# Kernel optimization log

Measured on AMD Instinct MI355X. Metric: run time of the kernel, lower is better.

Reference implementation:

```python
import jax, jax.numpy as jnp
import numpy as np
from jax import lax

NUM_HEADS = 4
OUT_DIM = 384
HEAD_DIM = 96
STRIDE_Q = 2
STRIDE_KV = 2
EPS = 1e-6
SCALE = HEAD_DIM ** -0.5


def _layernorm(x, g, b):
    m = jnp.mean(x, axis=-1, keepdims=True)
    v = jnp.mean((x - m) ** 2, axis=-1, keepdims=True)
    return (x - m) * lax.rsqrt(v + EPS) * g + b


def _pool(x, w, h, wd, stride):
    # x: [B, nh, N, hd] -> depthwise conv stride-s -> [B, nh, oh*ow, hd]
    B, nh, N, hd = x.shape
    x = x.reshape(B * nh, h, wd, hd).transpose(0, 3, 1, 2)  # NCHW
    y = lax.conv_general_dilated(x, w, (stride, stride), ((1, 1), (1, 1)),
                                 feature_group_count=hd)
    oh, ow = y.shape[2], y.shape[3]
    y = y.reshape(B, nh, hd, oh * ow).transpose(0, 1, 3, 2)
    return y, (oh, ow)


def _add_rel_pos(attn, q, q_size, k_size, rel_h, rel_w):
    qh, qw = q_size
    kh, kw = k_size
    B, nh, _, hd = q.shape
    qhr = max(kh / qh, 1.0); khr = max(qh / kh, 1.0)
    dh = (jnp.arange(qh)[:, None] * qhr - jnp.arange(kh)[None, :] * khr
          + (kh - 1) * khr).astype(jnp.int32)
    qwr = max(kw / qw, 1.0); kwr = max(qw / kw, 1.0)
    dw = (jnp.arange(qw)[:, None] * qwr - jnp.arange(kw)[None, :] * kwr
          + (kw - 1) * kwr).astype(jnp.int32)
    Reh = rel_h[dh]  # [qh, kh, hd]
    Rew = rel_w[dw]  # [qw, kw, hd]
    qr = q.reshape(B, nh, qh, qw, hd)
    eh = jnp.einsum('byhwc,hkc->byhwk', qr, Reh)
    ew = jnp.einsum('byhwc,wkc->byhwk', qr, Rew)
    a = attn.reshape(B, nh, qh, qw, kh, kw) + eh[..., :, None] + ew[..., None, :]
    return a.reshape(B, nh, qh * qw, kh * kw)


def setup_inputs() -> dict:
    key = jax.random.key(0)
    ks = jax.random.split(key, 8)
    B, N, IN_DIM = 16, 3136, 192
    return {
        'hidden_states': jax.random.normal(ks[0], (B, N, IN_DIM), jnp.float32),
        'qkv_w': jax.random.normal(ks[1], (IN_DIM, 3 * OUT_DIM), jnp.float32) * 0.02,
        'qkv_b': jax.random.normal(ks[2], (3 * OUT_DIM,), jnp.float32) * 0.02,
        'pool_q_w': jax.random.normal(ks[3], (HEAD_DIM, 1, 3, 3), jnp.float32) * 0.1,
        'pool_k_w': jax.random.normal(ks[4], (HEAD_DIM, 1, 3, 3), jnp.float32) * 0.1,
        'pool_v_w': jax.random.normal(ks[5], (HEAD_DIM, 1, 3, 3), jnp.float32) * 0.1,
        'ln_q_g': jnp.ones((HEAD_DIM,), jnp.float32),
        'ln_q_b': jnp.zeros((HEAD_DIM,), jnp.float32),
        'ln_k_g': jnp.ones((HEAD_DIM,), jnp.float32),
        'ln_k_b': jnp.zeros((HEAD_DIM,), jnp.float32),
        'ln_v_g': jnp.ones((HEAD_DIM,), jnp.float32),
        'ln_v_b': jnp.zeros((HEAD_DIM,), jnp.float32),
        'rel_h': jax.random.normal(ks[6], (55, HEAD_DIM), jnp.float32) * 0.02,
        'rel_w': jax.random.normal(ks[7], (55, HEAD_DIM), jnp.float32) * 0.02,
        'height': 56,
        'width': 56,
    }


def reference(hidden_states, qkv_w, qkv_b, pool_q_w, pool_k_w, pool_v_w,
              ln_q_g, ln_q_b, ln_k_g, ln_k_b, ln_v_g, ln_v_b,
              rel_h, rel_w, height, width):
    B, N, _ = hidden_states.shape
    qkv = (hidden_states @ qkv_w + qkv_b).reshape(B, N, 3, NUM_HEADS, HEAD_DIM)
    qkv = qkv.transpose(2, 0, 3, 1, 4)  # [3, B, nh, N, hd]
    q, k, v = qkv[0], qkv[1], qkv[2]

    q, q_size = _pool(q, pool_q_w, height, width, STRIDE_Q)
    q = _layernorm(q, ln_q_g, ln_q_b)
    k, k_size = _pool(k, pool_k_w, height, width, STRIDE_KV)
    k = _layernorm(k, ln_k_g, ln_k_b)
    v, _ = _pool(v, pool_v_w, height, width, STRIDE_KV)
    v = _layernorm(v, ln_v_g, ln_v_b)

    attn = jnp.einsum('bhqd,bhkd->bhqk', q * SCALE, k)
    attn = _add_rel_pos(attn, q, q_size, k_size, rel_h, rel_w)
    attn = jax.nn.softmax(attn, axis=-1)
    out = jnp.einsum('bhqk,bhkd->bhqd', attn, v)
    out = out + q  # residual pooling (no cls token)
    out = out.transpose(0, 2, 1, 3).reshape(B, -1, OUT_DIM)
    return out
```

## Files before the change

kernel.cpp:

```cpp
#include <hip/hip_runtime.h>

#define DEVI __device__ __forceinline__

typedef __attribute__((ext_vector_type(8))) short short8;
typedef __attribute__((ext_vector_type(4))) short short4v;
typedef __attribute__((ext_vector_type(4))) float f32x4;
typedef __attribute__((ext_vector_type(4))) unsigned int u32x4;

#define ATTN_SCALE 0.10206207261596575f
#define LOG2E      1.4426950408889634f
#define KSCALE     (ATTN_SCALE * LOG2E)

DEVI unsigned short f2bf(float f){
  unsigned u = __float_as_uint(f);
  u += 0x7fff + ((u >> 16) & 1);
  return (unsigned short)(u >> 16);
}
DEVI float bf2f(unsigned short h){ return __uint_as_float(((unsigned)h) << 16); }

DEVI void gload16(const void* g, void* l){
  __builtin_amdgcn_global_load_lds((const __attribute__((address_space(1))) void*)g,
                                   (__attribute__((address_space(3))) void*)l, 16, 0, 0);
}

DEVI f32x4 mfma16(short8 a, short8 b, f32x4 c){
  return __builtin_amdgcn_mfma_f32_16x16x32_bf16(a, b, c, 0, 0, 0);
}

DEVI short8 pack_bf8s(const float* p, float s){
  float4 a = *(const float4*)p, b = *(const float4*)(p + 4);
  short8 r;
  r[0] = f2bf(a.x * s); r[1] = f2bf(a.y * s); r[2] = f2bf(a.z * s); r[3] = f2bf(a.w * s);
  r[4] = f2bf(b.x * s); r[5] = f2bf(b.y * s); r[6] = f2bf(b.z * s); r[7] = f2bf(b.w * s);
  return r;
}

__global__ __launch_bounds__(256) void k_convert(const float4* __restrict__ hs4,
    const float* __restrict__ w, unsigned short* __restrict__ hsb,
    unsigned short* __restrict__ wt){
  const int stride = gridDim.x * 256;
  const int t0 = blockIdx.x * 256 + threadIdx.x;
  const int n4 = (50176 * 192) / 4;
  for (int i = t0; i < n4; i += stride){
    float4 v = hs4[i];
    uint2 p;
    p.x = (unsigned)f2bf(v.x) | ((unsigned)f2bf(v.y) << 16);
    p.y = (unsigned)f2bf(v.z) | ((unsigned)f2bf(v.w) << 16);
    ((uint2*)hsb)[i] = p;
  }
  for (int i = t0; i < 192 * 1152; i += stride){
    int k = i / 1152, n = i - k * 1152;
    wt[n * 192 + k] = f2bf(w[i]);
  }
}

__global__ __launch_bounds__(256) void k_gemm(const unsigned short* __restrict__ A,
    const unsigned short* __restrict__ Bt,
    const float* __restrict__ bias, unsigned short* __restrict__ C){
  __shared__ unsigned short sA[2][128 * 64];
  __shared__ unsigned short sB[2][128 * 64];
  const int bid = (blockIdx.x & 7) * 441 + (blockIdx.x >> 3);
  const int bn = bid % 9, bm = bid / 9;
  const int tid = threadIdx.x, w = tid >> 6, l = tid & 63;
  const int wr = (w >> 1) * 64, wc = (w & 1) * 64;
  const int l15 = l & 15, l4 = l >> 4;
  const f32x4 z4 = {0.f, 0.f, 0.f, 0.f};
  f32x4 acc[4][4];
#pragma unroll
  for (int i = 0; i < 4; ++i)
#pragma unroll
    for (int j = 0; j < 4; ++j) acc[i][j] = z4;

  auto stage = [&](int kk, int buf){
    const int k0 = kk * 64;
#pragma unroll
    for (int i = 0; i < 4; ++i){
      const int ib = (w * 4 + i) << 10;
      const int Lb = ib + (l << 4);
      const int r  = Lb >> 7;
      const int g  = ((Lb >> 4) & 7) ^ (r & 7);
      gload16((const char*)A  + (size_t)(bm * 128 + r) * 384 + k0 * 2 + g * 16, (char*)sA[buf] + ib);
      gload16((const char*)Bt + (size_t)(bn * 128 + r) * 384 + k0 * 2 + g * 16, (char*)sB[buf] + ib);
    }
  };

  stage(0, 0);
  __syncthreads();
  for (int kk = 0; kk < 3; ++kk){
    const int buf = kk & 1;
    if (kk < 2) stage(kk + 1, buf ^ 1);
#pragma unroll
    for (int ks = 0; ks < 2; ++ks){
      short8 av[4], bv[4];
#pragma unroll
      for (int mf = 0; mf < 4; ++mf){
        const int r = wr + mf * 16 + l15;
        const int slot = (ks * 4 + l4) ^ (r & 7);
        av[mf] = *(const short8*)(sA[buf] + r * 64 + slot * 8);
      }
#pragma unroll
      for (int nf = 0; nf < 4; ++nf){
        const int r = wc + nf * 16 + l15;
        const int slot = (ks * 4 + l4) ^ (r & 7);
        bv[nf] = *(const short8*)(sB[buf] + r * 64 + slot * 8);
      }
#pragma unroll
      for (int mf = 0; mf < 4; ++mf)
#pragma unroll
        for (int nf = 0; nf < 4; ++nf)
          acc[mf][nf] = mfma16(av[mf], bv[nf], acc[mf][nf]);
    }
    if (kk < 2) __syncthreads();
  }
#pragma unroll
  for (int nf = 0; nf < 4; ++nf){
    const int col = bn * 128 + wc + nf * 16 + l15;
    const float bv = bias[col];
#pragma unroll
    for (int mf = 0; mf < 4; ++mf)
#pragma unroll
      for (int reg = 0; reg < 4; ++reg){
        const int row = bm * 128 + wr + mf * 16 + l4 * 4 + reg;
        C[(size_t)row * 1152 + col] = f2bf(acc[mf][nf][reg] + bv);
      }
  }
}

__global__ __launch_bounds__(384) void k_pool_ln(const unsigned short* __restrict__ qkv,
    const float* __restrict__ wq, const float* __restrict__ wk, const float* __restrict__ wv,
    const float* __restrict__ gq, const float* __restrict__ bq,
    const float* __restrict__ gk, const float* __restrict__ bk,
    const float* __restrict__ gv, const float* __restrict__ bv,
    unsigned short* __restrict__ qp, unsigned short* __restrict__ kp,
    unsigned short* __restrict__ vpt, float* __restrict__ qpf){
  __shared__ float swt[9 * 96];
  __shared__ float sg[96], sb[96];
  __shared__ float sbuf[28 * 96];
  const int bid = blockIdx.x;
  const int oy = bid % 28, h = (bid / 28) & 3, b = (bid / 112) & 15, which = bid / 1792;
  const float* wsel = which == 0 ? wq : (which == 1 ? wk : wv);
  const float* gsel = which == 0 ? gq : (which == 1 ? gk : gv);
  const float* bsel = which == 0 ? bq : (which == 1 ? bk : bv);
  const int tid = threadIdx.x;
  for (int i = tid; i < 864; i += 384){
    const int d = i / 9, t = i - d * 9;
    swt[t * 96 + d] = wsel[i];
  }
  if (tid < 96){ sg[tid] = gsel[tid]; sb[tid] = bsel[tid]; }
  __syncthreads();

  const int colbase = which * 384 + h * 96;
  if (tid < 336){
    const int ox = tid / 12, d0 = (tid - ox * 12) * 8;
    float acc[8] = {0.f,0.f,0.f,0.f,0.f,0.f,0.f,0.f};
#pragma unroll
    for (int ky = 0; ky < 3; ++ky){
      const int iy = oy * 2 + ky - 1;
      if ((unsigned)iy >= 56u) continue;
      const unsigned short* rowp = qkv + (size_t)(b * 3136 + iy * 56) * 1152 + colbase + d0;
#pragma unroll
      for (int kx = 0; kx < 3; ++kx){
        const int ix = ox * 2 + kx - 1;
        if ((unsigned)ix >= 56u) continue;
        const u32x4 raw = *(const u32x4*)(rowp + (size_t)ix * 1152);
        const float* wv8 = swt + (ky * 3 + kx) * 96 + d0;
        const float4 wa = *(const float4*)wv8;
        const float4 wb = *(const float4*)(wv8 + 4);
        acc[0] += __uint_as_float(raw[0] << 16)         * wa.x;
        acc[1] += __uint_as_float(raw[0] & 0xffff0000u) * wa.y;
        acc[2] += __uint_as_float(raw[1] << 16)         * wa.z;
        acc[3] += __uint_as_float(raw[1] & 0xffff0000u) * wa.w;
        acc[4] += __uint_as_float(raw[2] << 16)         * wb.x;
        acc[5] += __uint_as_float(raw[2] & 0xffff0000u) * wb.y;
        acc[6] += __uint_as_float(raw[3] << 16)         * wb.z;
        acc[7] += __uint_as_float(raw[3] & 0xffff0000u) * wb.w;
      }
    }
    *(float4*)(sbuf + ox * 96 + d0)     = *(float4*)acc;
    *(float4*)(sbuf + ox * 96 + d0 + 4) = *(float4*)(acc + 4);
  }
  __syncthreads();

  const int grp = tid >> 3, l8 = tid & 7;
  if (grp < 28){
    const int ox = grp, d0 = l8 * 12;
    float x[12];
    *(float4*)x       = *(const float4*)(sbuf + ox * 96 + d0);
    *(float4*)(x + 4) = *(const float4*)(sbuf + ox * 96 + d0 + 4);
    *(float4*)(x + 8) = *(const float4*)(sbuf + ox * 96 + d0 + 8);
    float s = 0.f, ss = 0.f;
#pragma unroll
    for (int j = 0; j < 12; ++j){ s += x[j]; ss += x[j] * x[j]; }
#pragma unroll
    for (int d = 1; d < 8; d <<= 1){ s += __shfl_xor(s, d); ss += __shfl_xor(ss, d); }
    const float mean = s * (1.f / 96.f);
    const float var  = ss * (1.f / 96.f) - mean * mean;
    const float rstd = rsqrtf(var + 1e-6f);
    const int n = oy * 28 + ox;
    const size_t bh = (size_t)(b * 4 + h);
    float y[12];
#pragma unroll
    for (int j = 0; j < 12; ++j)
      y[j] = (x[j] - mean) * rstd * sg[d0 + j] + sb[d0 + j];
    if (which == 0){
      const size_t idx = (bh * 784 + n) * 96 + d0;
#pragma unroll
      for (int c = 0; c < 3; ++c){
        short4v p;
        p[0] = (short)f2bf(y[c*4]);   p[1] = (short)f2bf(y[c*4+1]);
        p[2] = (short)f2bf(y[c*4+2]); p[3] = (short)f2bf(y[c*4+3]);
        *(short4v*)(qp + idx + c * 4) = p;
        *(float4*)(qpf + idx + c * 4) = *(const float4*)(y + c * 4);
      }
    } else if (which == 1){
      const size_t idx = (bh * 784 + n) * 160;
#pragma unroll
      for (int c = 0; c < 3; ++c){
        short4v p;
        p[0] = (short)f2bf(y[c*4]   * KSCALE); p[1] = (short)f2bf(y[c*4+1] * KSCALE);
        p[2] = (short)f2bf(y[c*4+2] * KSCALE); p[3] = (short)f2bf(y[c*4+3] * KSCALE);
        *(short4v*)(kp + idx + d0 + c * 4) = p;
      }
      short8 oh;
#pragma unroll
      for (int jj = 0; jj < 8; ++jj){
        const int pcol = 96 + l8 * 8 + jj;
        unsigned short v = 0;
        if (pcol == 96 + oy)  v = 0x3F80;
        if (pcol == 128 + ox) v = 0x3F80;
        oh[jj] = (short)v;
      }
      *(short8*)(kp + idx + 96 + l8 * 8) = oh;
    } else {
#pragma unroll
      for (int j = 0; j < 12; ++j)
        vpt[(bh * 96 + d0 + j) * 784 + n] = f2bf(y[j]);
    }
  }
}

__global__ __launch_bounds__(512, 4) void k_attn(
    const unsigned short* __restrict__ qp, const unsigned short* __restrict__ kp,
    const unsigned short* __restrict__ vpt, const float* __restrict__ qpf,
    const float* __restrict__ relh, const float* __restrict__ relw,
    float* __restrict__ out){
  __shared__ unsigned short sK[2][64 * 160];
  __shared__ unsigned short sV[96 * 64];

  const int s = blockIdx.x, xcd = s & 7, slot = s >> 3;
  const int bh = xcd * 8 + slot / 7, qb = slot - (slot / 7) * 7;
  const int b = bh >> 2, h = bh & 3;
  const int tid = threadIdx.x, w = tid >> 6, l = tid & 63;
  const int l15 = l & 15, l4 = l >> 4;
  const size_t baseq = (size_t)bh * 784 * 96;
  const size_t basek = (size_t)bh * 784 * 160;
  const f32x4 z4 = {0.f, 0.f, 0.f, 0.f};
  const int qrl = w * 16 + l15;
  int q_l = qb * 128 + qrl; if (q_l > 783) q_l = 783;

  auto stageK = [&](int t, int buf){
#pragma unroll
    for (int r = 0; r < 3; ++r){
      if (r == 2 && tid >= 256) continue;
      const int off = r * 8192 + (tid << 4);
      const int row = ((off >> 6) * 205) >> 10;
      const int rem = off - row * 320;
      const int sg_ = (rem >> 4) ^ (row & 3);
      int kr = t * 64 + row; if (kr > 783) kr = 783;
      gload16((const char*)kp + ((size_t)(basek + (size_t)kr * 160) + sg_ * 8) * 2,
              (char*)sK[buf] + off);
    }
  };
  short8 vreg[2];
  auto loadV = [&](int t){
    if (tid < 384){
#pragma unroll
      for (int i = 0; i < 2; ++i){
        const int off = (tid * 2 + i) << 4;
        const int r = off >> 7;
        const int g = ((off >> 4) & 7) ^ (r & 7);
        int koff = t * 64 + g * 8; if (koff + 8 > 784) koff = 0;
        vreg[i] = *(const short8*)(vpt + (size_t)(bh * 96 + r) * 784 + koff);
      }
    }
  };
  auto writeV = [&](){
    if (tid < 384){
#pragma unroll
      for (int i = 0; i < 2; ++i)
        *(short8*)((char*)sV + ((tid * 2 + i) << 4)) = vreg[i];
    }
  };

  stageK(0, 0);
  loadV(0);

  short8 qf[5];
#pragma unroll
  for (int ks = 0; ks < 3; ++ks)
    qf[ks] = *(const short8*)(qp + baseq + (size_t)q_l * 96 + ks * 32 + l4 * 8);

  const int hh = (q_l * 2341) >> 16;
  const int ww = q_l - hh * 28;
  const int h0 = (qb * 128) / 28;

  {
    unsigned short* sGh = sK[1];
    unsigned short* sGw = sK[1] + 4096;
    f32x4 gh[3] = {z4, z4, z4}, gw[4] = {z4, z4, z4, z4};
#pragma unroll
    for (int nf = 0; nf < 3; ++nf){
      int j = h0 + nf * 16 + l15; if (j > 54) j = 54;
#pragma unroll
      for (int ks = 0; ks < 3; ++ks)
        gh[nf] = mfma16(pack_bf8s(relh + j * 96 + ks * 32 + l4 * 8, LOG2E), qf[ks], gh[nf]);
    }
#pragma unroll
    for (int nf = 0; nf < 4; ++nf){
      int j = nf * 16 + l15; if (j > 54) j = 54;
#pragma unroll
      for (int ks = 0; ks < 3; ++ks)
        gw[nf] = mfma16(pack_bf8s(relw + j * 96 + ks * 32 + l4 * 8, LOG2E), qf[ks], gw[nf]);
    }
    if (l4 == 0){
      *(short4v*)(sGh + qrl * 32 + 28) = (short4v)0;
      *(short4v*)(sGw + qrl * 32 + 28) = (short4v)0;
    }
#pragma unroll
    for (int nf = 0; nf < 3; ++nf)
#pragma unroll
      for (int reg = 0; reg < 4; ++reg){
        const int j = h0 + nf * 16 + l4 * 4 + reg;
        const int kh = hh + 27 - j;
        if ((unsigned)kh < 28u) sGh[qrl * 32 + kh] = f2bf(gh[nf][reg]);
      }
#pragma unroll
    for (int nf = 0; nf < 4; ++nf)
#pragma unroll
      for (int reg = 0; reg < 4; ++reg){
        const int j = nf * 16 + l4 * 4 + reg;
        const int kw = ww + 27 - j;
        if ((unsigned)kw < 28u) sGw[qrl * 32 + kw] = f2bf(gw[nf][reg]);
      }
    qf[3] = *(const short8*)(sGh + qrl * 32 + l4 * 8);
    qf[4] = *(const short8*)(sGw + qrl * 32 + l4 * 8);
  }

  float m = -1e30f, lsum = 0.f;
  f32x4 acc[6];
#pragma unroll
  for (int i = 0; i < 6; ++i) acc[i] = z4;

  writeV();
  __syncthreads();

  for (int kt = 0; kt < 13; ++kt){
    const int cur = kt & 1;
    if (kt < 12){ loadV(kt + 1); stageK(kt + 1, cur ^ 1); }

    f32x4 sfr[4] = {z4, z4, z4, z4};
#pragma unroll
    for (int ks = 0; ks < 5; ++ks){
#pragma unroll
      for (int nf = 0; nf < 4; ++nf){
        const int r = nf * 16 + l15;
        const int sl = (ks * 4 + l4) ^ (r & 3);
        const short8 kb = *(const short8*)(sK[cur] + r * 160 + sl * 8);
        sfr[nf] = mfma16(kb, qf[ks], sfr[nf]);
      }
    }
    if (kt == 12){
      const f32x4 m30 = {-1e30f, -1e30f, -1e30f, -1e30f};
      sfr[1] = m30; sfr[2] = m30; sfr[3] = m30;
    }

    float mx;
    {
      float a0 = fmaxf(fmaxf(sfr[0][0], sfr[0][1]), fmaxf(sfr[0][2], sfr[0][3]));
      float a1 = fmaxf(fmaxf(sfr[1][0], sfr[1][1]), fmaxf(sfr[1][2], sfr[1][3]));
      float a2 = fmaxf(fmaxf(sfr[2][0], sfr[2][1]), fmaxf(sfr[2][2], sfr[2][3]));
      float a3 = fmaxf(fmaxf(sfr[3][0], sfr[3][1]), fmaxf(sfr[3][2], sfr[3][3]));
      mx = fmaxf(fmaxf(a0, a1), fmaxf(a2, a3));
    }
    mx = fmaxf(mx, __shfl_xor(mx, 16));
    mx = fmaxf(mx, __shfl_xor(mx, 32));
    const float mn = fmaxf(m, mx);
    const float al = exp2f(m - mn);
    m = mn;
    float sum;
    {
#pragma unroll
      for (int nf = 0; nf < 4; ++nf)
#pragma unroll
        for (int reg = 0; reg < 4; ++reg)
          sfr[nf][reg] = exp2f(sfr[nf][reg] - mn);
      float s0 = (sfr[0][0] + sfr[0][1]) + (sfr[0][2] + sfr[0][3]);
      float s1 = (sfr[1][0] + sfr[1][1]) + (sfr[1][2] + sfr[1][3]);
      float s2 = (sfr[2][0] + sfr[2][1]) + (sfr[2][2] + sfr[2][3]);
      float s3 = (sfr[3][0] + sfr[3][1]) + (sfr[3][2] + sfr[3][3]);
      sum = (s0 + s1) + (s2 + s3);
    }
    sum += __shfl_xor(sum, 16);
    sum += __shfl_xor(sum, 32);
    lsum = lsum * al + sum;

    __syncthreads();

    unsigned short* sPp = sK[cur];
#pragma unroll
    for (int nf = 0; nf < 4; ++nf){
      short4v p4;
      p4[0] = (short)f2bf(sfr[nf][0]); p4[1] = (short)f2bf(sfr[nf][1]);
      p4[2] = (short)f2bf(sfr[nf][2]); p4[3] = (short)f2bf(sfr[nf][3]);
      char* dst = (char*)sPp + qrl * 128 + (((nf * 2 + (l4 >> 1)) ^ (l15 & 7)) << 4) + ((l4 & 1) << 3);
      *(short4v*)dst = p4;
    }
#pragma unroll
    for (int i = 0; i < 6; ++i)
#pragma unroll
      for (int reg = 0; reg < 4; ++reg)
        acc[i][reg] *= al;

#pragma unroll
    for (int ks = 0; ks < 2; ++ks){
      const short8 pb = *(const short8*)((char*)sPp + qrl * 128 + (((ks * 4 + l4) ^ (l15 & 7)) << 4));
#pragma unroll
      for (int nf = 0; nf < 6; ++nf){
        const int r = nf * 16 + l15;
        const int sl = (ks * 4 + l4) ^ (r & 7);
        const short8 vb = *(const short8*)(sV + r * 64 + sl * 8);
        acc[nf] = mfma16(vb, pb, acc[nf]);
      }
    }

    if (kt < 12){
      __syncthreads();
      writeV();
      __syncthreads();
    }
  }

  const int qg = qb * 128 + qrl;
  if (qg < 784){
    const float rcp = 1.f / lsum;
    const float* qrow = qpf + baseq + (size_t)qg * 96;
    float* orow = out + ((size_t)b * 784 + qg) * 384 + h * 96;
#pragma unroll
    for (int nf = 0; nf < 6; ++nf)
#pragma unroll
      for (int reg = 0; reg < 4; ++reg){
        const int d = nf * 16 + l4 * 4 + reg;
        orow[d] = acc[nf][reg] * rcp + qrow[d];
      }
  }
}

extern "C" void kernel_launch(void* const* d_in, const int* in_sizes, int n_in,
                              void* d_out, int out_size, void* d_ws, size_t ws_size,
                              hipStream_t stream){
  const float* hs  = (const float*)d_in[0];
  const float* qw  = (const float*)d_in[1];
  const float* qb  = (const float*)d_in[2];
  const float* pwq = (const float*)d_in[3];
  const float* pwk = (const float*)d_in[4];
  const float* pwv = (const float*)d_in[5];
  const float* gq  = (const float*)d_in[6];
  const float* bq  = (const float*)d_in[7];
  const float* gk  = (const float*)d_in[8];
  const float* bk  = (const float*)d_in[9];
  const float* gv  = (const float*)d_in[10];
  const float* bv  = (const float*)d_in[11];
  const float* rh  = (const float*)d_in[12];
  const float* rw  = (const float*)d_in[13];
  float* out = (float*)d_out;

  char* ws = (char*)d_ws;
  size_t off = 0;
  auto take = [&](size_t n)->char*{ char* p = ws + off; off += (n + 255) & ~(size_t)255; return p; };
  unsigned short* hsb = (unsigned short*)take((size_t)50176 * 192 * 2);
  unsigned short* wtb = (unsigned short*)take((size_t)1152 * 192 * 2);
  unsigned short* qkv = (unsigned short*)take((size_t)50176 * 1152 * 2);
  unsigned short* qpb = (unsigned short*)take((size_t)64 * 784 * 96 * 2);
  unsigned short* kpb = (unsigned short*)take((size_t)64 * 784 * 160 * 2);
  unsigned short* vpt = (unsigned short*)take((size_t)64 * 784 * 96 * 2);
  float* qpf          = (float*)take((size_t)64 * 784 * 96 * 4);

  hipLaunchKernelGGL(k_convert, dim3(1024), dim3(256), 0, stream,
                     (const float4*)hs, qw, hsb, wtb);
  hipLaunchKernelGGL(k_gemm, dim3(392 * 9), dim3(256), 0, stream, hsb, wtb, qb, qkv);
  hipLaunchKernelGGL(k_pool_ln, dim3(5376), dim3(384), 0, stream, qkv,
                     pwq, pwk, pwv, gq, bq, gk, bk, gv, bv, qpb, kpb, vpt, qpf);
  hipLaunchKernelGGL(k_attn, dim3(448), dim3(512), 0, stream,
                     qpb, kpb, vpt, qpf, rh, rw, out);
}
```

Baseline: 269.8 us.

## Split attention KV range across two blocks and merge with combine kernel

The attention kernel now splits the 13 key tiles into two halves (7 and 6 tiles), doubling the grid from 448 to 896 blocks. Each block writes unnormalized partial outputs plus its running max and sum into scratch that reuses the qkv buffer. A new combine kernel merges the two partials and adds the residual. The K tile in LDS is also split into a 128-column main part and a 32-column rel-pos part with new swizzles. The aim is more parallelism and better CU occupancy on a small grid, at the cost of an extra launch and extra partial-result traffic through global memory.

```diff
diff --git a/kernel.cpp b/kernel.cpp
--- a/kernel.cpp
+++ b/kernel.cpp
@@ -241,15 +241,17 @@
 
 __global__ __launch_bounds__(512, 4) void k_attn(
     const unsigned short* __restrict__ qp, const unsigned short* __restrict__ kp,
-    const unsigned short* __restrict__ vpt, const float* __restrict__ qpf,
+    const unsigned short* __restrict__ vpt,
     const float* __restrict__ relh, const float* __restrict__ relw,
-    float* __restrict__ out){
-  __shared__ unsigned short sK[2][64 * 160];
+    float* __restrict__ po, float2* __restrict__ pml){
+  __shared__ unsigned short sKm[2][64 * 128];
+  __shared__ unsigned short sKe[2][64 * 32];
   __shared__ unsigned short sV[96 * 64];
 
   const int s = blockIdx.x, xcd = s & 7, slot = s >> 3;
-  const int bh = xcd * 8 + slot / 7, qb = slot - (slot / 7) * 7;
-  const int b = bh >> 2, h = bh & 3;
+  const int bh = xcd * 8 + slot / 14;
+  const int rem = slot - (slot / 14) * 14;
+  const int qb = rem >> 1, kvh = rem & 1;
   const int tid = threadIdx.x, w = tid >> 6, l = tid & 63;
   const int l15 = l & 15, l4 = l >> 4;
   const size_t baseq = (size_t)bh * 784 * 96;
@@ -257,18 +259,28 @@
   const f32x4 z4 = {0.f, 0.f, 0.f, 0.f};
   const int qrl = w * 16 + l15;
   int q_l = qb * 128 + qrl; if (q_l > 783) q_l = 783;
+  const int t0 = kvh ? 7 : 0, t1 = kvh ? 13 : 7;
 
   auto stageK = [&](int t, int buf){
-#pragma unroll
-    for (int r = 0; r < 3; ++r){
-      if (r == 2 && tid >= 256) continue;
-      const int off = r * 8192 + (tid << 4);
-      const int row = ((off >> 6) * 205) >> 10;
-      const int rem = off - row * 320;
-      const int sg_ = (rem >> 4) ^ (row & 3);
-      int kr = t * 64 + row; if (kr > 783) kr = 783;
-      gload16((const char*)kp + ((size_t)(basek + (size_t)kr * 160) + sg_ * 8) * 2,
-              (char*)sK[buf] + off);
+    int krr = t * 64;
+#pragma unroll
+    for (int rd = 0; rd < 2; ++rd){
+      const int off = rd * 8192 + (tid << 4);
+      const int row = off >> 8;
+      const int gr  = (off >> 4) & 15;
+      const int sg_ = (gr & 8) | ((gr ^ row) & 7);
+      int kr = krr + row; if (kr > 783) kr = 783;
+      gload16((const char*)kp + ((size_t)kr * 160 + basek + sg_ * 8) * 2,
+              (char*)sKm[buf] + off);
+    }
+    if (tid < 256){
+      const int off = tid << 4;
+      const int row = off >> 6;
+      const int gr  = (off >> 4) & 3;
+      const int sg_ = (gr ^ (row >> 1)) & 3;
+      int kr = krr + row; if (kr > 783) kr = 783;
+      gload16((const char*)kp + ((size_t)kr * 160 + basek + 128 + sg_ * 8) * 2,
+              (char*)sKe[buf] + off);
     }
   };
   short8 vreg[2];
@@ -292,8 +304,8 @@
     }
   };
 
-  stageK(0, 0);
-  loadV(0);
+  stageK(t0, 0);
+  loadV(t0);
 
   short8 qf[5];
 #pragma unroll
@@ -305,8 +317,8 @@
   const int h0 = (qb * 128) / 28;
 
   {
-    unsigned short* sGh = sK[1];
-    unsigned short* sGw = sK[1] + 4096;
+    unsigned short* sGh = sKm[1];
+    unsigned short* sGw = sKm[1] + 4096;
     f32x4 gh[3] = {z4, z4, z4}, gw[4] = {z4, z4, z4, z4};
 #pragma unroll
     for (int nf = 0; nf < 3; ++nf){
@@ -354,22 +366,30 @@
   writeV();
   __syncthreads();
 
-  for (int kt = 0; kt < 13; ++kt){
-    const int cur = kt & 1;
-    if (kt < 12){ loadV(kt + 1); stageK(kt + 1, cur ^ 1); }
+  for (int t = t0; t < t1; ++t){
+    const int cur = (t - t0) & 1;
+    if (t + 1 < t1){ loadV(t + 1); stageK(t + 1, cur ^ 1); }
 
     f32x4 sfr[4] = {z4, z4, z4, z4};
 #pragma unroll
-    for (int ks = 0; ks < 5; ++ks){
+    for (int ks = 0; ks < 4; ++ks){
+      const int g = ks * 4 + l4;
 #pragma unroll
       for (int nf = 0; nf < 4; ++nf){
         const int r = nf * 16 + l15;
-        const int sl = (ks * 4 + l4) ^ (r & 3);
-        const short8 kb = *(const short8*)(sK[cur] + r * 160 + sl * 8);
+        const int sl = (g & 8) | ((g ^ r) & 7);
+        const short8 kb = *(const short8*)(sKm[cur] + r * 128 + sl * 8);
         sfr[nf] = mfma16(kb, qf[ks], sfr[nf]);
       }
     }
-    if (kt == 12){
+#pragma unroll
+    for (int nf = 0; nf < 4; ++nf){
+      const int r = nf * 16 + l15;
+      const int sl = (l4 ^ (r >> 1)) & 3;
+      const short8 kb = *(const short8*)(sKe[cur] + r * 32 + sl * 8);
+      sfr[nf] = mfma16(kb, qf[4], sfr[nf]);
+    }
+    if (t == 12){
       const f32x4 m30 = {-1e30f, -1e30f, -1e30f, -1e30f};
       sfr[1] = m30; sfr[2] = m30; sfr[3] = m30;
     }
@@ -406,7 +426,7 @@
 
     __syncthreads();
 
-    unsigned short* sPp = sK[cur];
+    unsigned short* sPp = sKm[cur];
 #pragma unroll
     for (int nf = 0; nf < 4; ++nf){
       short4v p4;
@@ -433,7 +453,7 @@
       }
     }
 
-    if (kt < 12){
+    if (t + 1 < t1){
       __syncthreads();
       writeV();
       __syncthreads();
@@ -442,17 +462,41 @@
 
   const int qg = qb * 128 + qrl;
   if (qg < 784){
-    const float rcp = 1.f / lsum;
-    const float* qrow = qpf + baseq + (size_t)qg * 96;
-    float* orow = out + ((size_t)b * 784 + qg) * 384 + h * 96;
+    const size_t row = (size_t)kvh * 64 * 784 + (size_t)bh * 784 + qg;
+    float* pob = po + row * 96;
 #pragma unroll
     for (int nf = 0; nf < 6; ++nf)
-#pragma unroll
-      for (int reg = 0; reg < 4; ++reg){
-        const int d = nf * 16 + l4 * 4 + reg;
-        orow[d] = acc[nf][reg] * rcp + qrow[d];
-      }
-  }
+      *(f32x4*)(pob + nf * 16 + l4 * 4) = acc[nf];
+    if (l4 == 0) pml[row] = make_float2(m, lsum);
+  }
+}
+
+__global__ __launch_bounds__(256) void k_comb(const float* __restrict__ po,
+    const float2* __restrict__ pml, const float* __restrict__ qpf,
+    float* __restrict__ out){
+  const int idx = blockIdx.x * 256 + threadIdx.x;
+  if (idx >= 64 * 784 * 24) return;
+  const int d4 = idx % 24;
+  const int t  = idx / 24;
+  const int q  = t % 784;
+  const int bh = t / 784;
+  const int b = bh >> 2, h = bh & 3;
+  const size_t row = (size_t)bh * 784 + q;
+  const float2 ml1 = pml[row];
+  const float2 ml2 = pml[(size_t)64 * 784 + row];
+  const float M = fmaxf(ml1.x, ml2.x);
+  const float w1 = exp2f(ml1.x - M), w2 = exp2f(ml2.x - M);
+  const float rden = 1.f / (ml1.y * w1 + ml2.y * w2);
+  const size_t obase = row * 96 + d4 * 4;
+  const float4 o1 = *(const float4*)(po + obase);
+  const float4 o2 = *(const float4*)(po + (size_t)64 * 784 * 96 + obase);
+  const float4 qr = *(const float4*)(qpf + obase);
+  float4 r;
+  r.x = (o1.x * w1 + o2.x * w2) * rden + qr.x;
+  r.y = (o1.y * w1 + o2.y * w2) * rden + qr.y;
+  r.z = (o1.z * w1 + o2.z * w2) * rden + qr.z;
+  r.w = (o1.w * w1 + o2.w * w2) * rden + qr.w;
+  *(float4*)(out + ((size_t)b * 784 + q) * 384 + h * 96 + d4 * 4) = r;
 }
 
 extern "C" void kernel_launch(void* const* d_in, const int* in_sizes, int n_in,
@@ -484,12 +528,16 @@
   unsigned short* kpb = (unsigned short*)take((size_t)64 * 784 * 160 * 2);
   unsigned short* vpt = (unsigned short*)take((size_t)64 * 784 * 96 * 2);
   float* qpf          = (float*)take((size_t)64 * 784 * 96 * 4);
+  float*  po  = (float*)qkv;
+  float2* pml = (float2*)(po + (size_t)2 * 64 * 784 * 96);
 
   hipLaunchKernelGGL(k_convert, dim3(1024), dim3(256), 0, stream,
                      (const float4*)hs, qw, hsb, wtb);
   hipLaunchKernelGGL(k_gemm, dim3(392 * 9), dim3(256), 0, stream, hsb, wtb, qb, qkv);
   hipLaunchKernelGGL(k_pool_ln, dim3(5376), dim3(384), 0, stream, qkv,
                      pwq, pwk, pwv, gq, bq, gk, bk, gv, bv, qpb, kpb, vpt, qpf);
-  hipLaunchKernelGGL(k_attn, dim3(448), dim3(512), 0, stream,
-                     qpb, kpb, vpt, qpf, rh, rw, out);
-}
+  hipLaunchKernelGGL(k_attn, dim3(896), dim3(512), 0, stream,
+                     qpb, kpb, vpt, rh, rw, po, pml);
+  hipLaunchKernelGGL(k_comb, dim3((64 * 784 * 24 + 255) / 256), dim3(256), 0, stream,
+                     po, pml, qpf, out);
+}
```

After: 296.0 us. 1.1x slower.

## Stage GEMM output through LDS for coalesced stores; split K tile; pre-convert rel-pos tables

Applied to the files above, without the earlier changes.

The GEMM epilogue now swaps the MFMA operands so each lane holds four consecutive columns. It writes bias-added bf16 results into swizzled shared memory and then emits coalesced 16-byte row stores, replacing scattered 2-byte global writes. The attention kernel splits the 160-wide K rows into a 128-wide main tile and a 32-wide extra tile with power-of-two swizzles, which simplifies the address math and aims to cut LDS bank conflicts. The rel-pos tables are converted to bf16 and prescaled by log2(e) once in the convert kernel instead of being packed per block. This adds extra LDS round trips and barriers in the GEMM epilogue.

```diff
diff --git a/kernel.cpp b/kernel.cpp
--- a/kernel.cpp
+++ b/kernel.cpp
@@ -27,17 +27,10 @@
   return __builtin_amdgcn_mfma_f32_16x16x32_bf16(a, b, c, 0, 0, 0);
 }
 
-DEVI short8 pack_bf8s(const float* p, float s){
-  float4 a = *(const float4*)p, b = *(const float4*)(p + 4);
-  short8 r;
-  r[0] = f2bf(a.x * s); r[1] = f2bf(a.y * s); r[2] = f2bf(a.z * s); r[3] = f2bf(a.w * s);
-  r[4] = f2bf(b.x * s); r[5] = f2bf(b.y * s); r[6] = f2bf(b.z * s); r[7] = f2bf(b.w * s);
-  return r;
-}
-
 __global__ __launch_bounds__(256) void k_convert(const float4* __restrict__ hs4,
-    const float* __restrict__ w, unsigned short* __restrict__ hsb,
-    unsigned short* __restrict__ wt){
+    const float* __restrict__ w, const float* __restrict__ rh, const float* __restrict__ rw,
+    unsigned short* __restrict__ hsb, unsigned short* __restrict__ wt,
+    unsigned short* __restrict__ rhb, unsigned short* __restrict__ rwb){
   const int stride = gridDim.x * 256;
   const int t0 = blockIdx.x * 256 + threadIdx.x;
   const int n4 = (50176 * 192) / 4;
@@ -51,6 +44,10 @@
   for (int i = t0; i < 192 * 1152; i += stride){
     int k = i / 1152, n = i - k * 1152;
     wt[n * 192 + k] = f2bf(w[i]);
+  }
+  for (int i = t0; i < 55 * 96; i += stride){
+    rhb[i] = f2bf(rh[i] * LOG2E);
+    rwb[i] = f2bf(rw[i] * LOG2E);
   }
 }
 
@@ -108,21 +105,36 @@
       for (int mf = 0; mf < 4; ++mf)
 #pragma unroll
         for (int nf = 0; nf < 4; ++nf)
-          acc[mf][nf] = mfma16(av[mf], bv[nf], acc[mf][nf]);
+          acc[mf][nf] = mfma16(bv[nf], av[mf], acc[mf][nf]);
     }
     if (kk < 2) __syncthreads();
   }
+
+  __syncthreads();
+  unsigned short* sC = (unsigned short*)sA;
 #pragma unroll
   for (int nf = 0; nf < 4; ++nf){
-    const int col = bn * 128 + wc + nf * 16 + l15;
-    const float bv = bias[col];
-#pragma unroll
-    for (int mf = 0; mf < 4; ++mf)
-#pragma unroll
-      for (int reg = 0; reg < 4; ++reg){
-        const int row = bm * 128 + wr + mf * 16 + l4 * 4 + reg;
-        C[(size_t)row * 1152 + col] = f2bf(acc[mf][nf][reg] + bv);
-      }
+    const int colq = wc + nf * 16 + l4 * 4;
+    const float4 b4 = *(const float4*)(bias + bn * 128 + colq);
+#pragma unroll
+    for (int mf = 0; mf < 4; ++mf){
+      const int row = wr + mf * 16 + l15;
+      short4v p;
+      p[0] = (short)f2bf(acc[mf][nf][0] + b4.x);
+      p[1] = (short)f2bf(acc[mf][nf][1] + b4.y);
+      p[2] = (short)f2bf(acc[mf][nf][2] + b4.z);
+      p[3] = (short)f2bf(acc[mf][nf][3] + b4.w);
+      const int slot = (colq >> 3) ^ (row & 7);
+      *(short4v*)(sC + row * 128 + slot * 8 + (colq & 7)) = p;
+    }
+  }
+  __syncthreads();
+#pragma unroll
+  for (int i = 0; i < 8; ++i){
+    const int row = i * 16 + w * 4 + l4;
+    const int slot = l15 ^ (row & 7);
+    const short8 v = *(const short8*)(sC + row * 128 + slot * 8);
+    *(short8*)(C + (size_t)(bm * 128 + row) * 1152 + bn * 128 + l15 * 8) = v;
   }
 }
 
@@ -242,9 +254,10 @@
 __global__ __launch_bounds__(512, 4) void k_attn(
     const unsigned short* __restrict__ qp, const unsigned short* __restrict__ kp,
     const unsigned short* __restrict__ vpt, const float* __restrict__ qpf,
-    const float* __restrict__ relh, const float* __restrict__ relw,
+    const unsigned short* __restrict__ rhb, const unsigned short* __restrict__ rwb,
     float* __restrict__ out){
-  __shared__ unsigned short sK[2][64 * 160];
+  __shared__ unsigned short sKm[2][64 * 128];
+  __shared__ unsigned short sKe[2][64 * 32];
   __shared__ unsigned short sV[96 * 64];
 
   const int s = blockIdx.x, xcd = s & 7, slot = s >> 3;
@@ -259,16 +272,25 @@
   int q_l = qb * 128 + qrl; if (q_l > 783) q_l = 783;
 
   auto stageK = [&](int t, int buf){
-#pragma unroll
-    for (int r = 0; r < 3; ++r){
-      if (r == 2 && tid >= 256) continue;
-      const int off = r * 8192 + (tid << 4);
-      const int row = ((off >> 6) * 205) >> 10;
-      const int rem = off - row * 320;
-      const int sg_ = (rem >> 4) ^ (row & 3);
-      int kr = t * 64 + row; if (kr > 783) kr = 783;
-      gload16((const char*)kp + ((size_t)(basek + (size_t)kr * 160) + sg_ * 8) * 2,
-              (char*)sK[buf] + off);
+    int krr = t * 64;
+#pragma unroll
+    for (int rd = 0; rd < 2; ++rd){
+      const int off = rd * 8192 + (tid << 4);
+      const int row = off >> 8;
+      const int gr  = (off >> 4) & 15;
+      const int sg_ = (gr & 8) | ((gr ^ row) & 7);
+      int kr = krr + row; if (kr > 783) kr = 783;
+      gload16((const char*)kp + ((size_t)kr * 160 + basek + sg_ * 8) * 2,
+              (char*)sKm[buf] + off);
+    }
+    if (tid < 256){
+      const int off = tid << 4;
+      const int row = off >> 6;
+      const int gr  = (off >> 4) & 3;
+      const int sg_ = (gr ^ (row >> 1)) & 3;
+      int kr = krr + row; if (kr > 783) kr = 783;
+      gload16((const char*)kp + ((size_t)kr * 160 + basek + 128 + sg_ * 8) * 2,
+              (char*)sKe[buf] + off);
     }
   };
   short8 vreg[2];
@@ -305,22 +327,22 @@
   const int h0 = (qb * 128) / 28;
 
   {
-    unsigned short* sGh = sK[1];
-    unsigned short* sGw = sK[1] + 4096;
+    unsigned short* sGh = sKm[1];
+    unsigned short* sGw = sKm[1] + 4096;
     f32x4 gh[3] = {z4, z4, z4}, gw[4] = {z4, z4, z4, z4};
 #pragma unroll
     for (int nf = 0; nf < 3; ++nf){
       int j = h0 + nf * 16 + l15; if (j > 54) j = 54;
 #pragma unroll
       for (int ks = 0; ks < 3; ++ks)
-        gh[nf] = mfma16(pack_bf8s(relh + j * 96 + ks * 32 + l4 * 8, LOG2E), qf[ks], gh[nf]);
+        gh[nf] = mfma16(*(const short8*)(rhb + j * 96 + ks * 32 + l4 * 8), qf[ks], gh[nf]);
     }
 #pragma unroll
     for (int nf = 0; nf < 4; ++nf){
       int j = nf * 16 + l15; if (j > 54) j = 54;
 #pragma unroll
       for (int ks = 0; ks < 3; ++ks)
-        gw[nf] = mfma16(pack_bf8s(relw + j * 96 + ks * 32 + l4 * 8, LOG2E), qf[ks], gw[nf]);
+        gw[nf] = mfma16(*(const short8*)(rwb + j * 96 + ks * 32 + l4 * 8), qf[ks], gw[nf]);
     }
     if (l4 == 0){
       *(short4v*)(sGh + qrl * 32 + 28) = (short4v)0;
@@ -360,14 +382,22 @@
 
     f32x4 sfr[4] = {z4, z4, z4, z4};
 #pragma unroll
-    for (int ks = 0; ks < 5; ++ks){
+    for (int ks = 0; ks < 4; ++ks){
+      const int g = ks * 4 + l4;
 #pragma unroll
       for (int nf = 0; nf < 4; ++nf){
         const int r = nf * 16 + l15;
-        const int sl = (ks * 4 + l4) ^ (r & 3);
-        const short8 kb = *(const short8*)(sK[cur] + r * 160 + sl * 8);
+        const int sl = (g & 8) | ((g ^ r) & 7);
+        const short8 kb = *(const short8*)(sKm[cur] + r * 128 + sl * 8);
         sfr[nf] = mfma16(kb, qf[ks], sfr[nf]);
       }
+    }
+#pragma unroll
+    for (int nf = 0; nf < 4; ++nf){
+      const int r = nf * 16 + l15;
+      const int sl = (l4 ^ (r >> 1)) & 3;
+      const short8 kb = *(const short8*)(sKe[cur] + r * 32 + sl * 8);
+      sfr[nf] = mfma16(kb, qf[4], sfr[nf]);
     }
     if (kt == 12){
       const f32x4 m30 = {-1e30f, -1e30f, -1e30f, -1e30f};
@@ -406,7 +436,7 @@
 
     __syncthreads();
 
-    unsigned short* sPp = sK[cur];
+    unsigned short* sPp = sKm[cur];
 #pragma unroll
     for (int nf = 0; nf < 4; ++nf){
       short4v p4;
@@ -484,12 +514,14 @@
   unsigned short* kpb = (unsigned short*)take((size_t)64 * 784 * 160 * 2);
   unsigned short* vpt = (unsigned short*)take((size_t)64 * 784 * 96 * 2);
   float* qpf          = (float*)take((size_t)64 * 784 * 96 * 4);
+  unsigned short* rhb = (unsigned short*)take((size_t)55 * 96 * 2);
+  unsigned short* rwb = (unsigned short*)take((size_t)55 * 96 * 2);
 
   hipLaunchKernelGGL(k_convert, dim3(1024), dim3(256), 0, stream,
-                     (const float4*)hs, qw, hsb, wtb);
+                     (const float4*)hs, qw, rh, rw, hsb, wtb, rhb, rwb);
   hipLaunchKernelGGL(k_gemm, dim3(392 * 9), dim3(256), 0, stream, hsb, wtb, qb, qkv);
   hipLaunchKernelGGL(k_pool_ln, dim3(5376), dim3(384), 0, stream, qkv,
                      pwq, pwk, pwv, gq, bq, gk, bk, gv, bv, qpb, kpb, vpt, qpf);
   hipLaunchKernelGGL(k_attn, dim3(448), dim3(512), 0, stream,
-                     qpb, kpb, vpt, qpf, rh, rw, out);
-}
+                     qpb, kpb, vpt, qpf, rhb, rwb, out);
+}
```

Measured after the change: 259.6 us. 3.8% less time.
